# Optimization experiments

Measured on AMD Instinct MI355X. Metric: run time of the kernel, lower is better.

## Reference

```python
import math
import jax, jax.numpy as jnp
import numpy as np

D, NH, NL, NP = 256, 8, 3, 4
HD = D // NH
SHAPES = np.array([[92, 92], [46, 46], [23, 23]], dtype=np.int32)
LSI = np.concatenate([[0], np.cumsum(SHAPES[:, 0] * SHAPES[:, 1])[:-1]]).astype(np.int32)
LV = int((SHAPES[:, 0] * SHAPES[:, 1]).sum())  # 11109
B, LQ = 2, LV


def setup_inputs() -> dict:
    key = jax.random.key(0)
    ks = jax.random.split(key, 8)
    query = jax.random.normal(ks[0], (B, LQ, D), jnp.float32)
    reference_points = jax.random.uniform(ks[1], (B, LQ, NL, 2), dtype=jnp.float32)
    value_flat = jax.random.normal(ks[2], (B, LV, D), jnp.float32)
    # sampling_offsets: small random weight + structured directional bias (as in _reset_parameters)
    W_off = jax.random.normal(ks[3], (D, NH * NL * NP * 2), jnp.float32) * 0.01
    thetas = np.arange(NH, dtype=np.float64) * (2.0 * math.pi / NH)
    g = np.stack([np.cos(thetas), np.sin(thetas)], axis=-1)
    g = g / np.abs(g).max(axis=-1, keepdims=True)
    g = np.tile(g[:, None, None, :], (1, NL, NP, 1))
    g = g * (np.arange(NP) + 1)[None, None, :, None]
    b_off = jnp.asarray(g.reshape(-1), jnp.float32)
    W_attn = jax.random.normal(ks[4], (D, NH * NL * NP), jnp.float32) * 0.01
    b_attn = jnp.zeros((NH * NL * NP,), jnp.float32)
    W_val = jax.random.normal(ks[5], (D, D), jnp.float32) * (1.0 / math.sqrt(D))
    b_val = jnp.zeros((D,), jnp.float32)
    W_out = jax.random.normal(ks[6], (D, D), jnp.float32) * (1.0 / math.sqrt(D))
    b_out = jnp.zeros((D,), jnp.float32)
    return dict(query=query, reference_points=reference_points, value_flat=value_flat,
                W_val=W_val, b_val=b_val, W_off=W_off, b_off=b_off,
                W_attn=W_attn, b_attn=b_attn, W_out=W_out, b_out=b_out,
                spatial_shapes=jnp.asarray(SHAPES), level_start_index=jnp.asarray(LSI))


def _bilinear_sample(val_l, grid):
    """torch.F.grid_sample(mode='bilinear', padding_mode='zeros', align_corners=False).
    val_l: [B,H,W,nH,hd]; grid: [B,Q,nH,P,2] with (x,y) in [-1,1].
    Returns [B,nH,Q,P,hd]."""
    Bq, H, W, nH, hd = val_l.shape
    Q, P = grid.shape[1], grid.shape[3]
    x = ((grid[..., 0] + 1.0) * W - 1.0) * 0.5   # pixel coords, align_corners=False
    y = ((grid[..., 1] + 1.0) * H - 1.0) * 0.5
    x0f, y0f = jnp.floor(x), jnp.floor(y)
    lx, ly = x - x0f, y - y0f
    x0, y0 = x0f.astype(jnp.int32), y0f.astype(jnp.int32)
    val_bh = val_l.transpose(0, 3, 1, 2, 4).reshape(Bq * nH, H * W, hd)

    def corner(yi, xi, w):
        valid = (xi >= 0) & (xi < W) & (yi >= 0) & (yi < H)
        idx = jnp.clip(yi, 0, H - 1) * W + jnp.clip(xi, 0, W - 1)   # [B,Q,nH,P]
        idx_bh = idx.transpose(0, 2, 1, 3).reshape(Bq * nH, Q * P)
        g = jnp.take_along_axis(val_bh, idx_bh[:, :, None], axis=1)  # [B*nH, Q*P, hd]
        wm = (w * valid.astype(w.dtype)).transpose(0, 2, 1, 3).reshape(Bq * nH, Q * P, 1)
        return g * wm

    out = (corner(y0, x0, (1 - ly) * (1 - lx)) + corner(y0, x0 + 1, (1 - ly) * lx)
           + corner(y0 + 1, x0, ly * (1 - lx)) + corner(y0 + 1, x0 + 1, ly * lx))
    return out.reshape(Bq, nH, Q, P, hd)


def reference(query, reference_points, value_flat, W_val, b_val, W_off, b_off,
              W_attn, b_attn, W_out, b_out, spatial_shapes, level_start_index):
    shapes = np.asarray(spatial_shapes)          # static level geometry
    starts = np.asarray(level_start_index)
    Bq, Lq, _ = query.shape
    value = (value_flat @ W_val + b_val).reshape(Bq, -1, NH, HD)
    off = (query @ W_off + b_off).reshape(Bq, Lq, NH, NL, NP, 2)        # (dy,dx) pixels
    aw = jax.nn.softmax((query @ W_attn + b_attn).reshape(Bq, Lq, NH, NL * NP), axis=-1)
    aw = aw.reshape(Bq, Lq, NH, NL, NP)
    sh_f = jnp.asarray(shapes, jnp.float32)                              # [L,2] = (H,W)
    norm_off = off / sh_f[None, None, None, :, None, :]
    loc = reference_points[:, :, None, :, None, :] + norm_off           # [B,Lq,NH,NL,NP,2] (y,x)
    grid = 2.0 * loc[..., ::-1] - 1.0                                    # (x,y) in [-1,1]
    out = jnp.zeros((Bq, Lq, NH, HD), query.dtype)
    for l in range(NL):
        H, W = int(shapes[l, 0]), int(shapes[l, 1])
        s = int(starts[l])
        val_l = value[:, s:s + H * W].reshape(Bq, H, W, NH, HD)
        sampled = _bilinear_sample(val_l, grid[:, :, :, l])              # [B,NH,Lq,NP,HD]
        out = out + jnp.einsum('bhqpc,bqhp->bqhc', sampled, aw[:, :, :, l])
    return out.reshape(Bq, Lq, D) @ W_out + b_out
```

## Files before the change

### kernel.cpp

```cpp
#include <hip/hip_runtime.h>

#define LQn   11109
#define MTOT  22218

typedef __attribute__((ext_vector_type(8))) short short8;
typedef __attribute__((ext_vector_type(4))) float f32x4;

__device__ __forceinline__ unsigned short f2bf(float f) {
  union { float f; unsigned int u; } v; v.f = f;
  unsigned int r = v.u + 0x7fffu + ((v.u >> 16) & 1u);
  return (unsigned short)(r >> 16);
}

__global__ __launch_bounds__(256) void prep_weights(
    const float* __restrict__ Wval, const float* __restrict__ Woff,
    const float* __restrict__ Wattn, const float* __restrict__ Wout,
    const float* __restrict__ boff, const float* __restrict__ battn,
    unsigned short* __restrict__ Wval_t, unsigned short* __restrict__ Wcat_t,
    unsigned short* __restrict__ Wout_t, float* __restrict__ bcat) {
  int i = blockIdx.x * 256 + threadIdx.x;
  int n = i >> 8, k = i & 255;
  if (n < 256) {
    Wval_t[i] = f2bf(Wval[k * 256 + n]);
    Wout_t[i] = f2bf(Wout[k * 256 + n]);
  }
  float src = (n < 192) ? Woff[k * 192 + n] : Wattn[k * 96 + (n - 192)];
  Wcat_t[i] = f2bf(src);
  if (i < 288) bcat[i] = (i < 192) ? boff[i] : battn[i - 192];
}

__global__ __launch_bounds__(256) void gemm_fused12(
    const float* __restrict__ Aval,
    const float* __restrict__ Aq,
    const unsigned short* __restrict__ Bval,
    const unsigned short* __restrict__ Bcat,
    const float* __restrict__ bval, const float* __restrict__ bcat,
    unsigned short* __restrict__ value16,
    float* __restrict__ logits) {
  __shared__ unsigned short As[64][40];
  __shared__ unsigned short Bs[64][40];

  const int bm = blockIdx.x;
  int bn = blockIdx.y;
  const bool is2 = bn >= 4;
  if (is2) bn -= 4;
  const float* __restrict__ A = is2 ? Aq : Aval;
  const unsigned short* __restrict__ Bt = is2 ? Bcat : Bval;
  const float* __restrict__ bias = is2 ? bcat : bval;
  const int N = is2 ? 288 : 256;

  const int t = threadIdx.x;
  const int wave = t >> 6, lane = t & 63;
  const int wm = wave >> 1, wn = wave & 1;
  const int quad = lane >> 4, l16 = lane & 15;

  const int ldr = t >> 2;
  const int ldk = (t & 3) * 8;
  const int arow = bm * 64 + ldr;
  const int brow = bn * 64 + ldr;

  f32x4 acc[2][2];
  for (int i = 0; i < 2; i++)
    for (int j = 0; j < 2; j++) acc[i][j] = (f32x4){0.f, 0.f, 0.f, 0.f};

  for (int kb = 0; kb < 8; kb++) {
    const int k0 = kb * 32;
    float4 a0 = {0.f, 0.f, 0.f, 0.f}, a1 = a0;
    uint4 bv = {0u, 0u, 0u, 0u};
    if (arow < MTOT) {
      a0 = *(const float4*)(A + (size_t)arow * 256 + k0 + ldk);
      a1 = *(const float4*)(A + (size_t)arow * 256 + k0 + ldk + 4);
    }
    if (brow < N) bv = *(const uint4*)(Bt + (size_t)brow * 256 + k0 + ldk);
    ushort4 lo, hi;
    lo.x = f2bf(a0.x); lo.y = f2bf(a0.y); lo.z = f2bf(a0.z); lo.w = f2bf(a0.w);
    hi.x = f2bf(a1.x); hi.y = f2bf(a1.y); hi.z = f2bf(a1.z); hi.w = f2bf(a1.w);
    __syncthreads();
    *(ushort4*)(&As[ldr][ldk]) = lo;
    *(ushort4*)(&As[ldr][ldk + 4]) = hi;
    *(uint4*)(&Bs[ldr][ldk]) = bv;
    __syncthreads();
    short8 af[2], bfr[2];
    for (int i = 0; i < 2; i++)
      af[i] = *(const short8*)(&As[wm * 32 + i * 16 + l16][quad * 8]);
    for (int j = 0; j < 2; j++)
      bfr[j] = *(const short8*)(&Bs[wn * 32 + j * 16 + l16][quad * 8]);
    for (int i = 0; i < 2; i++)
      for (int j = 0; j < 2; j++)
        acc[i][j] = __builtin_amdgcn_mfma_f32_16x16x32_bf16(af[i], bfr[j], acc[i][j], 0, 0, 0);
  }

  for (int i = 0; i < 2; i++)
    for (int j = 0; j < 2; j++) {
      int colg = bn * 64 + wn * 32 + j * 16 + l16;
      if (colg >= N) continue;
      float bsv = bias[colg];
      int row0 = bm * 64 + wm * 32 + i * 16 + quad * 4;
      for (int r = 0; r < 4; r++) {
        int rg = row0 + r;
        if (rg >= MTOT) continue;
        float v = acc[i][j][r] + bsv;
        if (is2) {
          logits[(size_t)rg * 288 + colg] = v;
        } else {
          int b = (rg >= LQn) ? 1 : 0;
          int p = rg - b * LQn;
          value16[((size_t)(b * 8 + (colg >> 5)) * LQn + p) * 32 + (colg & 31)] = f2bf(v);
        }
      }
    }
}

__global__ __launch_bounds__(256) void gemm_a16(
    const unsigned short* __restrict__ A,
    const unsigned short* __restrict__ Bt,
    const float* __restrict__ bias,
    float* __restrict__ C) {
  __shared__ unsigned short As[64][40];
  __shared__ unsigned short Bs[64][40];

  const int t = threadIdx.x;
  const int bm = blockIdx.x, bn = blockIdx.y;
  const int wave = t >> 6, lane = t & 63;
  const int wm = wave >> 1, wn = wave & 1;
  const int quad = lane >> 4, l16 = lane & 15;

  const int ldr = t >> 2;
  const int ldk = (t & 3) * 8;
  const int arow = bm * 64 + ldr;
  const int brow = bn * 64 + ldr;

  f32x4 acc[2][2];
  for (int i = 0; i < 2; i++)
    for (int j = 0; j < 2; j++) acc[i][j] = (f32x4){0.f, 0.f, 0.f, 0.f};

  for (int kb = 0; kb < 8; kb++) {
    const int k0 = kb * 32;
    uint4 av = {0u, 0u, 0u, 0u}, bv = {0u, 0u, 0u, 0u};
    if (arow < MTOT) av = *(const uint4*)(A + (size_t)arow * 256 + k0 + ldk);
    bv = *(const uint4*)(Bt + (size_t)brow * 256 + k0 + ldk);
    __syncthreads();
    *(uint4*)(&As[ldr][ldk]) = av;
    *(uint4*)(&Bs[ldr][ldk]) = bv;
    __syncthreads();
    short8 af[2], bfr[2];
    for (int i = 0; i < 2; i++)
      af[i] = *(const short8*)(&As[wm * 32 + i * 16 + l16][quad * 8]);
    for (int j = 0; j < 2; j++)
      bfr[j] = *(const short8*)(&Bs[wn * 32 + j * 16 + l16][quad * 8]);
    for (int i = 0; i < 2; i++)
      for (int j = 0; j < 2; j++)
        acc[i][j] = __builtin_amdgcn_mfma_f32_16x16x32_bf16(af[i], bfr[j], acc[i][j], 0, 0, 0);
  }

  for (int i = 0; i < 2; i++)
    for (int j = 0; j < 2; j++) {
      int colg = bn * 64 + wn * 32 + j * 16 + l16;
      float bsv = bias[colg];
      int row0 = bm * 64 + wm * 32 + i * 16 + quad * 4;
      for (int r = 0; r < 4; r++) {
        int rg = row0 + r;
        if (rg < MTOT) C[(size_t)rg * 256 + colg] = acc[i][j][r] + bsv;
      }
    }
}

__global__ __launch_bounds__(256) void msda_sample4(
    const unsigned short* __restrict__ value16,
    const float* __restrict__ logits,
    const float* __restrict__ refp,
    unsigned short* __restrict__ sampled) {
  __shared__ float          tw[8][96][4];
  __shared__ unsigned short ti[8][96][4];
  __shared__ float hmx[8][8], hrd[8][8];
  __shared__ float rfs[8][6];

  const int t = threadIdx.x;
  const int qbase = blockIdx.x * 8;

  if (t < 48) {
    int q = t / 6;
    if (qbase + q < MTOT) rfs[q][t - q * 6] = refp[(size_t)qbase * 6 + t];
  }
  if (t >= 64 && t < 128) {
    int tt = t - 64;
    int q = tt >> 3, h = tt & 7;
    int bq = qbase + q;
    if (bq < MTOT) {
      const float* lrow = logits + (size_t)bq * 288 + 192 + h * 12;
      float mx = -1e30f;
#pragma unroll
      for (int i = 0; i < 12; i++) mx = fmaxf(mx, lrow[i]);
      float den = 0.f;
#pragma unroll
      for (int i = 0; i < 12; i++) den += __expf(lrow[i] - mx);
      hmx[q][h] = mx;
      hrd[q][h] = 1.0f / den;
    }
  }
  __syncthreads();

  {
    const int Hs[3] = {92, 46, 23};
    const int Ss[3] = {0, 8464, 10580};
#pragma unroll
    for (int r = 0; r < 3; r++) {
      const int task = t + r * 256;
      const int q = task / 96, s = task - q * 96;
      const int bq = qbase + q;
      if (bq < MTOT) {
        const int h = s / 12, pl = s - h * 12;
        const int l = pl >> 2;
        const int H = Hs[l], W = Hs[l], S = Ss[l];
        const float* lrow = logits + (size_t)bq * 288;
        const float aw = __expf(lrow[192 + s] - hmx[q][h]) * hrd[q][h];
        const float offy = lrow[2 * s], offx = lrow[2 * s + 1];
        const float x = rfs[q][l * 2 + 1] * W + offx - 0.5f;
        const float y = rfs[q][l * 2 + 0] * H + offy - 0.5f;
        const float xf = floorf(x), yf = floorf(y);
        const int x0 = (int)xf, y0 = (int)yf;
        const float lx = x - xf, ly = y - yf;
        const bool xv0 = (x0 >= 0) & (x0 < W), xv1 = (x0 + 1 >= 0) & (x0 + 1 < W);
        const bool yv0 = (y0 >= 0) & (y0 < H), yv1 = (y0 + 1 >= 0) & (y0 + 1 < H);
        const int xc0 = min(max(x0, 0), W - 1), xc1 = min(max(x0 + 1, 0), W - 1);
        const int yc0 = min(max(y0, 0), H - 1), yc1 = min(max(y0 + 1, 0), H - 1);
        const int slot = pl * 8 + h;
        ti[q][slot][0] = (unsigned short)(S + yc0 * W + xc0);
        ti[q][slot][1] = (unsigned short)(S + yc0 * W + xc1);
        ti[q][slot][2] = (unsigned short)(S + yc1 * W + xc0);
        ti[q][slot][3] = (unsigned short)(S + yc1 * W + xc1);
        tw[q][slot][0] = (yv0 & xv0) ? aw * (1.f - ly) * (1.f - lx) : 0.f;
        tw[q][slot][1] = (yv0 & xv1) ? aw * (1.f - ly) * lx : 0.f;
        tw[q][slot][2] = (yv1 & xv0) ? aw * ly * (1.f - lx) : 0.f;
        tw[q][slot][3] = (yv1 & xv1) ? aw * ly * lx : 0.f;
      }
    }
  }
  __syncthreads();

  {
    const int w = t >> 6, lane = t & 63;
    const int q = w * 2 + (lane >> 5);
    const int h = (lane >> 2) & 7, cg = lane & 3;
    const int bq = qbase + q;
    const bool qv = bq < MTOT;
    const int bqc = qv ? bq : 0;
    const char* __restrict__ vb =
        (const char*)value16 + (size_t)(bqc / LQn) * ((size_t)LQn * 512);
    const unsigned laneoff = (unsigned)h * (LQn * 64u) + (unsigned)cg * 16u;

    float a0 = 0.f, a1 = 0.f, a2 = 0.f, a3 = 0.f;
    float a4 = 0.f, a5 = 0.f, a6 = 0.f, a7 = 0.f;
#pragma unroll
    for (int p = 0; p < 12; p++) {
      const int slot = p * 8 + h;
      const ushort4 tiv = *(const ushort4*)(&ti[q][slot][0]);
      const f32x4 wv = *(const f32x4*)(&tw[q][slot][0]);
#pragma unroll
      for (int k = 0; k < 4; k++) {
        const unsigned pix =
            (k == 0) ? tiv.x : (k == 1) ? tiv.y : (k == 2) ? tiv.z : tiv.w;
        const float wgt = wv[k];
        const uint4 u = *(const uint4*)(vb + ((pix << 6) + laneoff));
        a0 += wgt * __uint_as_float(u.x << 16);
        a1 += wgt * __uint_as_float(u.x & 0xffff0000u);
        a2 += wgt * __uint_as_float(u.y << 16);
        a3 += wgt * __uint_as_float(u.y & 0xffff0000u);
        a4 += wgt * __uint_as_float(u.z << 16);
        a5 += wgt * __uint_as_float(u.z & 0xffff0000u);
        a6 += wgt * __uint_as_float(u.w << 16);
        a7 += wgt * __uint_as_float(u.w & 0xffff0000u);
      }
    }
    if (qv) {
      uint4 o;
      o.x = (unsigned)f2bf(a0) | ((unsigned)f2bf(a1) << 16);
      o.y = (unsigned)f2bf(a2) | ((unsigned)f2bf(a3) << 16);
      o.z = (unsigned)f2bf(a4) | ((unsigned)f2bf(a5) << 16);
      o.w = (unsigned)f2bf(a6) | ((unsigned)f2bf(a7) << 16);
      *(uint4*)(sampled + (size_t)bq * 256 + h * 32 + cg * 8) = o;
    }
  }
}

extern "C" void kernel_launch(void* const* d_in, const int* in_sizes, int n_in,
                              void* d_out, int out_size, void* d_ws, size_t ws_size,
                              hipStream_t stream) {
  const float* query      = (const float*)d_in[0];
  const float* refp       = (const float*)d_in[1];
  const float* value_flat = (const float*)d_in[2];
  const float* W_val      = (const float*)d_in[3];
  const float* b_val      = (const float*)d_in[4];
  const float* W_off      = (const float*)d_in[5];
  const float* b_off      = (const float*)d_in[6];
  const float* W_attn     = (const float*)d_in[7];
  const float* b_attn     = (const float*)d_in[8];
  const float* W_out      = (const float*)d_in[9];
  const float* b_out      = (const float*)d_in[10];

  char* w = (char*)d_ws;
  size_t o = 0;
  auto carve = [&](size_t bytes) -> void* {
    void* p = (void*)(w + o);
    o += (bytes + 255) & ~(size_t)255;
    return p;
  };
  unsigned short* Wval_t  = (unsigned short*)carve(256 * 256 * 2);
  unsigned short* Wcat_t  = (unsigned short*)carve(288 * 256 * 2);
  unsigned short* Wout_t  = (unsigned short*)carve(256 * 256 * 2);
  float*          bcat    = (float*)carve(288 * 4);
  unsigned short* value16 = (unsigned short*)carve((size_t)MTOT * 256 * 2);
  float*          logits  = (float*)carve((size_t)MTOT * 288 * 4);
  unsigned short* samp_bf = (unsigned short*)carve((size_t)MTOT * 256 * 2);

  prep_weights<<<288, 256, 0, stream>>>(W_val, W_off, W_attn, W_out, b_off, b_attn,
                                        Wval_t, Wcat_t, Wout_t, bcat);

  const int mg = (MTOT + 63) / 64;
  dim3 g12(mg, 9);
  gemm_fused12<<<g12, 256, 0, stream>>>(value_flat, query, Wval_t, Wcat_t,
                                        b_val, bcat, value16, logits);

  const int sgrid = (MTOT + 7) / 8;
  msda_sample4<<<sgrid, 256, 0, stream>>>(value16, logits, refp, samp_bf);

  dim3 g3(mg, 4);
  gemm_a16<<<g3, 256, 0, stream>>>(samp_bf, Wout_t, b_out, (float*)d_out);
}
```

Before: 192.1 us.

## Keep A tile resident in LDS and loop over N blocks; remap sampler blocks per XCD

```diff
diff --git a/kernel.cpp b/kernel.cpp
--- a/kernel.cpp
+++ b/kernel.cpp
@@ -37,18 +37,17 @@
     const float* __restrict__ bval, const float* __restrict__ bcat,
     unsigned short* __restrict__ value16,
     float* __restrict__ logits) {
-  __shared__ unsigned short As[64][40];
+  __shared__ unsigned short As[8][64][40];
   __shared__ unsigned short Bs[64][40];
 
-  const int bm = blockIdx.x;
-  int bn = blockIdx.y;
-  const bool is2 = bn >= 4;
-  if (is2) bn -= 4;
+  const bool is2 = blockIdx.y == 1;
   const float* __restrict__ A = is2 ? Aq : Aval;
   const unsigned short* __restrict__ Bt = is2 ? Bcat : Bval;
   const float* __restrict__ bias = is2 ? bcat : bval;
   const int N = is2 ? 288 : 256;
-
+  const int NB = is2 ? 5 : 4;
+
+  const int bm = blockIdx.x;
   const int t = threadIdx.x;
   const int wave = t >> 6, lane = t & 63;
   const int wm = wave >> 1, wn = wave & 1;
@@ -57,58 +56,62 @@
   const int ldr = t >> 2;
   const int ldk = (t & 3) * 8;
   const int arow = bm * 64 + ldr;
-  const int brow = bn * 64 + ldr;
-
-  f32x4 acc[2][2];
-  for (int i = 0; i < 2; i++)
-    for (int j = 0; j < 2; j++) acc[i][j] = (f32x4){0.f, 0.f, 0.f, 0.f};
 
   for (int kb = 0; kb < 8; kb++) {
-    const int k0 = kb * 32;
     float4 a0 = {0.f, 0.f, 0.f, 0.f}, a1 = a0;
-    uint4 bv = {0u, 0u, 0u, 0u};
     if (arow < MTOT) {
-      a0 = *(const float4*)(A + (size_t)arow * 256 + k0 + ldk);
-      a1 = *(const float4*)(A + (size_t)arow * 256 + k0 + ldk + 4);
-    }
-    if (brow < N) bv = *(const uint4*)(Bt + (size_t)brow * 256 + k0 + ldk);
+      a0 = *(const float4*)(A + (size_t)arow * 256 + kb * 32 + ldk);
+      a1 = *(const float4*)(A + (size_t)arow * 256 + kb * 32 + ldk + 4);
+    }
     ushort4 lo, hi;
     lo.x = f2bf(a0.x); lo.y = f2bf(a0.y); lo.z = f2bf(a0.z); lo.w = f2bf(a0.w);
     hi.x = f2bf(a1.x); hi.y = f2bf(a1.y); hi.z = f2bf(a1.z); hi.w = f2bf(a1.w);
-    __syncthreads();
-    *(ushort4*)(&As[ldr][ldk]) = lo;
-    *(ushort4*)(&As[ldr][ldk + 4]) = hi;
-    *(uint4*)(&Bs[ldr][ldk]) = bv;
-    __syncthreads();
-    short8 af[2], bfr[2];
+    *(ushort4*)(&As[kb][ldr][ldk]) = lo;
+    *(ushort4*)(&As[kb][ldr][ldk + 4]) = hi;
+  }
+
+  for (int bn = 0; bn < NB; bn++) {
+    const int brow = bn * 64 + ldr;
+    f32x4 acc[2][2];
     for (int i = 0; i < 2; i++)
-      af[i] = *(const short8*)(&As[wm * 32 + i * 16 + l16][quad * 8]);
-    for (int j = 0; j < 2; j++)
-      bfr[j] = *(const short8*)(&Bs[wn * 32 + j * 16 + l16][quad * 8]);
+      for (int j = 0; j < 2; j++) acc[i][j] = (f32x4){0.f, 0.f, 0.f, 0.f};
+
+    for (int kb = 0; kb < 8; kb++) {
+      uint4 bv = {0u, 0u, 0u, 0u};
+      if (brow < N) bv = *(const uint4*)(Bt + (size_t)brow * 256 + kb * 32 + ldk);
+      __syncthreads();
+      *(uint4*)(&Bs[ldr][ldk]) = bv;
+      __syncthreads();
+      short8 af[2], bfr[2];
+      for (int i = 0; i < 2; i++)
+        af[i] = *(const short8*)(&As[kb][wm * 32 + i * 16 + l16][quad * 8]);
+      for (int j = 0; j < 2; j++)
+        bfr[j] = *(const short8*)(&Bs[wn * 32 + j * 16 + l16][quad * 8]);
+      for (int i = 0; i < 2; i++)
+        for (int j = 0; j < 2; j++)
+          acc[i][j] = __builtin_amdgcn_mfma_f32_16x16x32_bf16(af[i], bfr[j], acc[i][j], 0, 0, 0);
+    }
+
     for (int i = 0; i < 2; i++)
-      for (int j = 0; j < 2; j++)
-        acc[i][j] = __builtin_amdgcn_mfma_f32_16x16x32_bf16(af[i], bfr[j], acc[i][j], 0, 0, 0);
-  }
-
-  for (int i = 0; i < 2; i++)
-    for (int j = 0; j < 2; j++) {
-      int colg = bn * 64 + wn * 32 + j * 16 + l16;
-      if (colg >= N) continue;
-      float bsv = bias[colg];
-      int row0 = bm * 64 + wm * 32 + i * 16 + quad * 4;
-      for (int r = 0; r < 4; r++) {
-        int rg = row0 + r;
-        if (rg >= MTOT) continue;
-        float v = acc[i][j][r] + bsv;
-        if (is2) {
-          logits[(size_t)rg * 288 + colg] = v;
-        } else {
-          int b = (rg >= LQn) ? 1 : 0;
-          int p = rg - b * LQn;
-          value16[((size_t)(b * 8 + (colg >> 5)) * LQn + p) * 32 + (colg & 31)] = f2bf(v);
+      for (int j = 0; j < 2; j++) {
+        int colg = bn * 64 + wn * 32 + j * 16 + l16;
+        if (colg >= N) continue;
+        float bsv = bias[colg];
+        int row0 = bm * 64 + wm * 32 + i * 16 + quad * 4;
+        for (int r = 0; r < 4; r++) {
+          int rg = row0 + r;
+          if (rg >= MTOT) continue;
+          float v = acc[i][j][r] + bsv;
+          if (is2) {
+            logits[(size_t)rg * 288 + colg] = v;
+          } else {
+            int b = (rg >= LQn) ? 1 : 0;
+            int p = rg - b * LQn;
+            value16[((size_t)(b * 8 + (colg >> 5)) * LQn + p) * 32 + (colg & 31)] = f2bf(v);
+          }
         }
       }
-    }
+  }
 }
 
 __global__ __launch_bounds__(256) void gemm_a16(
@@ -116,11 +119,11 @@
     const unsigned short* __restrict__ Bt,
     const float* __restrict__ bias,
     float* __restrict__ C) {
-  __shared__ unsigned short As[64][40];
+  __shared__ unsigned short As[8][64][40];
   __shared__ unsigned short Bs[64][40];
 
   const int t = threadIdx.x;
-  const int bm = blockIdx.x, bn = blockIdx.y;
+  const int bm = blockIdx.x;
   const int wave = t >> 6, lane = t & 63;
   const int wm = wave >> 1, wn = wave & 1;
   const int quad = lane >> 4, l16 = lane & 15;
@@ -128,41 +131,45 @@
   const int ldr = t >> 2;
   const int ldk = (t & 3) * 8;
   const int arow = bm * 64 + ldr;
-  const int brow = bn * 64 + ldr;
-
-  f32x4 acc[2][2];
-  for (int i = 0; i < 2; i++)
-    for (int j = 0; j < 2; j++) acc[i][j] = (f32x4){0.f, 0.f, 0.f, 0.f};
 
   for (int kb = 0; kb < 8; kb++) {
-    const int k0 = kb * 32;
-    uint4 av = {0u, 0u, 0u, 0u}, bv = {0u, 0u, 0u, 0u};
-    if (arow < MTOT) av = *(const uint4*)(A + (size_t)arow * 256 + k0 + ldk);
-    bv = *(const uint4*)(Bt + (size_t)brow * 256 + k0 + ldk);
-    __syncthreads();
-    *(uint4*)(&As[ldr][ldk]) = av;
-    *(uint4*)(&Bs[ldr][ldk]) = bv;
-    __syncthreads();
-    short8 af[2], bfr[2];
+    uint4 av = {0u, 0u, 0u, 0u};
+    if (arow < MTOT) av = *(const uint4*)(A + (size_t)arow * 256 + kb * 32 + ldk);
+    *(uint4*)(&As[kb][ldr][ldk]) = av;
+  }
+
+  for (int bn = 0; bn < 4; bn++) {
+    const int brow = bn * 64 + ldr;
+    f32x4 acc[2][2];
     for (int i = 0; i < 2; i++)
-      af[i] = *(const short8*)(&As[wm * 32 + i * 16 + l16][quad * 8]);
-    for (int j = 0; j < 2; j++)
-      bfr[j] = *(const short8*)(&Bs[wn * 32 + j * 16 + l16][quad * 8]);
+      for (int j = 0; j < 2; j++) acc[i][j] = (f32x4){0.f, 0.f, 0.f, 0.f};
+
+    for (int kb = 0; kb < 8; kb++) {
+      uint4 bv = *(const uint4*)(Bt + (size_t)brow * 256 + kb * 32 + ldk);
+      __syncthreads();
+      *(uint4*)(&Bs[ldr][ldk]) = bv;
+      __syncthreads();
+      short8 af[2], bfr[2];
+      for (int i = 0; i < 2; i++)
+        af[i] = *(const short8*)(&As[kb][wm * 32 + i * 16 + l16][quad * 8]);
+      for (int j = 0; j < 2; j++)
+        bfr[j] = *(const short8*)(&Bs[wn * 32 + j * 16 + l16][quad * 8]);
+      for (int i = 0; i < 2; i++)
+        for (int j = 0; j < 2; j++)
+          acc[i][j] = __builtin_amdgcn_mfma_f32_16x16x32_bf16(af[i], bfr[j], acc[i][j], 0, 0, 0);
+    }
+
     for (int i = 0; i < 2; i++)
-      for (int j = 0; j < 2; j++)
-        acc[i][j] = __builtin_amdgcn_mfma_f32_16x16x32_bf16(af[i], bfr[j], acc[i][j], 0, 0, 0);
-  }
-
-  for (int i = 0; i < 2; i++)
-    for (int j = 0; j < 2; j++) {
-      int colg = bn * 64 + wn * 32 + j * 16 + l16;
-      float bsv = bias[colg];
-      int row0 = bm * 64 + wm * 32 + i * 16 + quad * 4;
-      for (int r = 0; r < 4; r++) {
-        int rg = row0 + r;
-        if (rg < MTOT) C[(size_t)rg * 256 + colg] = acc[i][j][r] + bsv;
+      for (int j = 0; j < 2; j++) {
+        int colg = bn * 64 + wn * 32 + j * 16 + l16;
+        float bsv = bias[colg];
+        int row0 = bm * 64 + wm * 32 + i * 16 + quad * 4;
+        for (int r = 0; r < 4; r++) {
+          int rg = row0 + r;
+          if (rg < MTOT) C[(size_t)rg * 256 + colg] = acc[i][j][r] + bsv;
+        }
       }
-    }
+  }
 }
 
 __global__ __launch_bounds__(256) void msda_sample4(
@@ -176,7 +183,13 @@
   __shared__ float rfs[8][6];
 
   const int t = threadIdx.x;
-  const int qbase = blockIdx.x * 8;
+
+  const int nwg = gridDim.x;
+  const int xcd = blockIdx.x & 7;
+  const int pos = blockIdx.x >> 3;
+  const int qch = nwg >> 3, rch = nwg & 7;
+  const int nbid = xcd * qch + min(xcd, rch) + pos;
+  const int qbase = nbid * 8;
 
   if (t < 48) {
     int q = t / 6;
@@ -317,13 +330,12 @@
                                         Wval_t, Wcat_t, Wout_t, bcat);
 
   const int mg = (MTOT + 63) / 64;
-  dim3 g12(mg, 9);
+  dim3 g12(mg, 2);
   gemm_fused12<<<g12, 256, 0, stream>>>(value_flat, query, Wval_t, Wcat_t,
                                         b_val, bcat, value16, logits);
 
   const int sgrid = (MTOT + 7) / 8;
   msda_sample4<<<sgrid, 256, 0, stream>>>(value16, logits, refp, samp_bf);
 
-  dim3 g3(mg, 4);
-  gemm_a16<<<g3, 256, 0, stream>>>(samp_bf, Wout_t, b_out, (float*)d_out);
-}
+  gemm_a16<<<mg, 256, 0, stream>>>(samp_bf, Wout_t, b_out, (float*)d_out);
+}
```

New measurement: 195.8 us. No clear change (+1.9%).

## Drop LDS staging in GEMMs, load MFMA fragments directly, add XCD-aware block swizzle

Applied to the files above, without the earlier changes.

```diff
diff --git a/kernel.cpp b/kernel.cpp
--- a/kernel.cpp
+++ b/kernel.cpp
@@ -10,6 +10,21 @@
   union { float f; unsigned int u; } v; v.f = f;
   unsigned int r = v.u + 0x7fffu + ((v.u >> 16) & 1u);
   return (unsigned short)(r >> 16);
+}
+
+__device__ __forceinline__ short8 cvt8(float4 a, float4 b) {
+  short8 s;
+  s[0] = (short)f2bf(a.x); s[1] = (short)f2bf(a.y);
+  s[2] = (short)f2bf(a.z); s[3] = (short)f2bf(a.w);
+  s[4] = (short)f2bf(b.x); s[5] = (short)f2bf(b.y);
+  s[6] = (short)f2bf(b.z); s[7] = (short)f2bf(b.w);
+  return s;
+}
+
+__device__ __forceinline__ int xcd_swz(int bid, int nwg) {
+  const int xcd = bid & 7, pos = bid >> 3;
+  const int q = nwg >> 3, r = nwg & 7;
+  return (xcd < r ? xcd * (q + 1) : r * (q + 1) + (xcd - r) * q) + pos;
 }
 
 __global__ __launch_bounds__(256) void prep_weights(
@@ -37,13 +52,11 @@
     const float* __restrict__ bval, const float* __restrict__ bcat,
     unsigned short* __restrict__ value16,
     float* __restrict__ logits) {
-  __shared__ unsigned short As[64][40];
-  __shared__ unsigned short Bs[64][40];
-
-  const int bm = blockIdx.x;
-  int bn = blockIdx.y;
-  const bool is2 = bn >= 4;
-  if (is2) bn -= 4;
+  const int lb = xcd_swz(blockIdx.x, gridDim.x);
+  const int strip = lb / 9;
+  const int cg = lb - strip * 9;
+  const bool is2 = cg >= 4;
+  const int n0 = (is2 ? cg - 4 : cg) * 64;
   const float* __restrict__ A = is2 ? Aq : Aval;
   const unsigned short* __restrict__ Bt = is2 ? Bcat : Bval;
   const float* __restrict__ bias = is2 ? bcat : bval;
@@ -51,60 +64,68 @@
 
   const int t = threadIdx.x;
   const int wave = t >> 6, lane = t & 63;
-  const int wm = wave >> 1, wn = wave & 1;
   const int quad = lane >> 4, l16 = lane & 15;
-
-  const int ldr = t >> 2;
-  const int ldk = (t & 3) * 8;
-  const int arow = bm * 64 + ldr;
-  const int brow = bn * 64 + ldr;
-
-  f32x4 acc[2][2];
-  for (int i = 0; i < 2; i++)
-    for (int j = 0; j < 2; j++) acc[i][j] = (f32x4){0.f, 0.f, 0.f, 0.f};
-
+  const int m0 = strip * 128 + wave * 32;
+
+  const int r0 = m0 + l16, r1 = m0 + 16 + l16;
+  const bool av0 = r0 < MTOT, av1 = r1 < MTOT;
+  const float* ap0 = A + (size_t)r0 * 256 + quad * 8;
+  const float* ap1 = A + (size_t)r1 * 256 + quad * 8;
+
+  const unsigned short* bp[4];
+  bool bv[4];
+#pragma unroll
+  for (int nf = 0; nf < 4; nf++) {
+    const int col = n0 + nf * 16 + l16;
+    bv[nf] = col < N;
+    bp[nf] = Bt + (size_t)col * 256 + quad * 8;
+  }
+
+  f32x4 acc[2][4];
+#pragma unroll
+  for (int mf = 0; mf < 2; mf++)
+#pragma unroll
+    for (int nf = 0; nf < 4; nf++) acc[mf][nf] = (f32x4){0.f, 0.f, 0.f, 0.f};
+
+  const float4 z4 = {0.f, 0.f, 0.f, 0.f};
+#pragma unroll 2
   for (int kb = 0; kb < 8; kb++) {
-    const int k0 = kb * 32;
-    float4 a0 = {0.f, 0.f, 0.f, 0.f}, a1 = a0;
-    uint4 bv = {0u, 0u, 0u, 0u};
-    if (arow < MTOT) {
-      a0 = *(const float4*)(A + (size_t)arow * 256 + k0 + ldk);
-      a1 = *(const float4*)(A + (size_t)arow * 256 + k0 + ldk + 4);
-    }
-    if (brow < N) bv = *(const uint4*)(Bt + (size_t)brow * 256 + k0 + ldk);
-    ushort4 lo, hi;
-    lo.x = f2bf(a0.x); lo.y = f2bf(a0.y); lo.z = f2bf(a0.z); lo.w = f2bf(a0.w);
-    hi.x = f2bf(a1.x); hi.y = f2bf(a1.y); hi.z = f2bf(a1.z); hi.w = f2bf(a1.w);
-    __syncthreads();
-    *(ushort4*)(&As[ldr][ldk]) = lo;
-    *(ushort4*)(&As[ldr][ldk + 4]) = hi;
-    *(uint4*)(&Bs[ldr][ldk]) = bv;
-    __syncthreads();
-    short8 af[2], bfr[2];
-    for (int i = 0; i < 2; i++)
-      af[i] = *(const short8*)(&As[wm * 32 + i * 16 + l16][quad * 8]);
-    for (int j = 0; j < 2; j++)
-      bfr[j] = *(const short8*)(&Bs[wn * 32 + j * 16 + l16][quad * 8]);
-    for (int i = 0; i < 2; i++)
-      for (int j = 0; j < 2; j++)
-        acc[i][j] = __builtin_amdgcn_mfma_f32_16x16x32_bf16(af[i], bfr[j], acc[i][j], 0, 0, 0);
-  }
-
-  for (int i = 0; i < 2; i++)
-    for (int j = 0; j < 2; j++) {
-      int colg = bn * 64 + wn * 32 + j * 16 + l16;
+    const int ko = kb * 32;
+    float4 x0 = av0 ? *(const float4*)(ap0 + ko) : z4;
+    float4 x1 = av0 ? *(const float4*)(ap0 + ko + 4) : z4;
+    float4 y0 = av1 ? *(const float4*)(ap1 + ko) : z4;
+    float4 y1 = av1 ? *(const float4*)(ap1 + ko + 4) : z4;
+    short8 bfr[4];
+#pragma unroll
+    for (int nf = 0; nf < 4; nf++)
+      bfr[nf] = bv[nf] ? *(const short8*)(bp[nf] + ko) : (short8){0,0,0,0,0,0,0,0};
+    const short8 a0 = cvt8(x0, x1);
+    const short8 a1 = cvt8(y0, y1);
+#pragma unroll
+    for (int nf = 0; nf < 4; nf++) {
+      acc[0][nf] = __builtin_amdgcn_mfma_f32_16x16x32_bf16(a0, bfr[nf], acc[0][nf], 0, 0, 0);
+      acc[1][nf] = __builtin_amdgcn_mfma_f32_16x16x32_bf16(a1, bfr[nf], acc[1][nf], 0, 0, 0);
+    }
+  }
+
+#pragma unroll
+  for (int mf = 0; mf < 2; mf++)
+#pragma unroll
+    for (int nf = 0; nf < 4; nf++) {
+      const int colg = n0 + nf * 16 + l16;
       if (colg >= N) continue;
-      float bsv = bias[colg];
-      int row0 = bm * 64 + wm * 32 + i * 16 + quad * 4;
+      const float bsv = bias[colg];
+      const int row0 = m0 + mf * 16 + quad * 4;
+#pragma unroll
       for (int r = 0; r < 4; r++) {
-        int rg = row0 + r;
+        const int rg = row0 + r;
         if (rg >= MTOT) continue;
-        float v = acc[i][j][r] + bsv;
+        const float v = acc[mf][nf][r] + bsv;
         if (is2) {
           logits[(size_t)rg * 288 + colg] = v;
         } else {
-          int b = (rg >= LQn) ? 1 : 0;
-          int p = rg - b * LQn;
+          const int b = (rg >= LQn) ? 1 : 0;
+          const int p = rg - b * LQn;
           value16[((size_t)(b * 8 + (colg >> 5)) * LQn + p) * 32 + (colg & 31)] = f2bf(v);
         }
       }
@@ -116,53 +137,51 @@
     const unsigned short* __restrict__ Bt,
     const float* __restrict__ bias,
     float* __restrict__ C) {
-  __shared__ unsigned short As[64][40];
-  __shared__ unsigned short Bs[64][40];
+  const int lb = xcd_swz(blockIdx.x, gridDim.x);
+  const int strip = lb >> 2;
+  const int n0 = (lb & 3) * 64;
 
   const int t = threadIdx.x;
-  const int bm = blockIdx.x, bn = blockIdx.y;
   const int wave = t >> 6, lane = t & 63;
-  const int wm = wave >> 1, wn = wave & 1;
   const int quad = lane >> 4, l16 = lane & 15;
-
-  const int ldr = t >> 2;
-  const int ldk = (t & 3) * 8;
-  const int arow = bm * 64 + ldr;
-  const int brow = bn * 64 + ldr;
-
-  f32x4 acc[2][2];
-  for (int i = 0; i < 2; i++)
-    for (int j = 0; j < 2; j++) acc[i][j] = (f32x4){0.f, 0.f, 0.f, 0.f};
-
+  const int m0 = strip * 64 + wave * 16;
+
+  const int r0 = m0 + l16;
+  const bool av0 = r0 < MTOT;
+  const unsigned short* ap = A + (size_t)r0 * 256 + quad * 8;
+
+  const unsigned short* bp[4];
+#pragma unroll
+  for (int nf = 0; nf < 4; nf++)
+    bp[nf] = Bt + (size_t)(n0 + nf * 16 + l16) * 256 + quad * 8;
+
+  f32x4 acc[4];
+#pragma unroll
+  for (int nf = 0; nf < 4; nf++) acc[nf] = (f32x4){0.f, 0.f, 0.f, 0.f};
+
+#pragma unroll 2
   for (int kb = 0; kb < 8; kb++) {
-    const int k0 = kb * 32;
-    uint4 av = {0u, 0u, 0u, 0u}, bv = {0u, 0u, 0u, 0u};
-    if (arow < MTOT) av = *(const uint4*)(A + (size_t)arow * 256 + k0 + ldk);
-    bv = *(const uint4*)(Bt + (size_t)brow * 256 + k0 + ldk);
-    __syncthreads();
-    *(uint4*)(&As[ldr][ldk]) = av;
-    *(uint4*)(&Bs[ldr][ldk]) = bv;
-    __syncthreads();
-    short8 af[2], bfr[2];
-    for (int i = 0; i < 2; i++)
-      af[i] = *(const short8*)(&As[wm * 32 + i * 16 + l16][quad * 8]);
-    for (int j = 0; j < 2; j++)
-      bfr[j] = *(const short8*)(&Bs[wn * 32 + j * 16 + l16][quad * 8]);
-    for (int i = 0; i < 2; i++)
-      for (int j = 0; j < 2; j++)
-        acc[i][j] = __builtin_amdgcn_mfma_f32_16x16x32_bf16(af[i], bfr[j], acc[i][j], 0, 0, 0);
-  }
-
-  for (int i = 0; i < 2; i++)
-    for (int j = 0; j < 2; j++) {
-      int colg = bn * 64 + wn * 32 + j * 16 + l16;
-      float bsv = bias[colg];
-      int row0 = bm * 64 + wm * 32 + i * 16 + quad * 4;
-      for (int r = 0; r < 4; r++) {
-        int rg = row0 + r;
-        if (rg < MTOT) C[(size_t)rg * 256 + colg] = acc[i][j][r] + bsv;
-      }
-    }
+    const int ko = kb * 32;
+    const short8 a0 = av0 ? *(const short8*)(ap + ko) : (short8){0,0,0,0,0,0,0,0};
+    short8 bfr[4];
+#pragma unroll
+    for (int nf = 0; nf < 4; nf++) bfr[nf] = *(const short8*)(bp[nf] + ko);
+#pragma unroll
+    for (int nf = 0; nf < 4; nf++)
+      acc[nf] = __builtin_amdgcn_mfma_f32_16x16x32_bf16(a0, bfr[nf], acc[nf], 0, 0, 0);
+  }
+
+#pragma unroll
+  for (int nf = 0; nf < 4; nf++) {
+    const int colg = n0 + nf * 16 + l16;
+    const float bsv = bias[colg];
+    const int row0 = m0 + quad * 4;
+#pragma unroll
+    for (int r = 0; r < 4; r++) {
+      const int rg = row0 + r;
+      if (rg < MTOT) C[(size_t)rg * 256 + colg] = acc[nf][r] + bsv;
+    }
+  }
 }
 
 __global__ __launch_bounds__(256) void msda_sample4(
@@ -176,7 +195,8 @@
   __shared__ float rfs[8][6];
 
   const int t = threadIdx.x;
-  const int qbase = blockIdx.x * 8;
+  const int nbid = xcd_swz(blockIdx.x, gridDim.x);
+  const int qbase = nbid * 8;
 
   if (t < 48) {
     int q = t / 6;
@@ -316,14 +336,13 @@
   prep_weights<<<288, 256, 0, stream>>>(W_val, W_off, W_attn, W_out, b_off, b_attn,
                                         Wval_t, Wcat_t, Wout_t, bcat);
 
-  const int mg = (MTOT + 63) / 64;
-  dim3 g12(mg, 9);
-  gemm_fused12<<<g12, 256, 0, stream>>>(value_flat, query, Wval_t, Wcat_t,
-                                        b_val, bcat, value16, logits);
+  const int mg128 = (MTOT + 127) / 128;
+  gemm_fused12<<<mg128 * 9, 256, 0, stream>>>(value_flat, query, Wval_t, Wcat_t,
+                                              b_val, bcat, value16, logits);
 
   const int sgrid = (MTOT + 7) / 8;
   msda_sample4<<<sgrid, 256, 0, stream>>>(value16, logits, refp, samp_bf);
 
-  dim3 g3(mg, 4);
-  gemm_a16<<<g3, 256, 0, stream>>>(samp_bf, Wout_t, b_out, (float*)d_out);
-}
+  const int mg64 = (MTOT + 63) / 64;
+  gemm_a16<<<mg64 * 4, 256, 0, stream>>>(samp_bf, Wout_t, b_out, (float*)d_out);
+}
```

New measurement: 300.3 us. 1.56x slower.
